# Performance work log

Measured on AMD Instinct MI355X. Metric: run time of the kernel, lower is better.

Reference implementation:

```python
import jax, jax.numpy as jnp
import numpy as np

N, E, D = 20000, 160000, 128   # nodes, edges, d_model
GH, HC = 4, 128                # TransformerConv heads, per-head channels (= out_channels)
MH = 4                         # temporal MHA heads
MC = D // MH                   # temporal MHA per-head dim
EPS = 1e-5


def layer_norm(x, g, b):
    mu = x.mean(-1, keepdims=True)
    var = ((x - mu) ** 2).mean(-1, keepdims=True)
    return (x - mu) * jax.lax.rsqrt(var + EPS) * g + b


def forward(x, temporal_encoding, gq_w, gq_b, gk_w, gk_b, gv_w, gv_b, gs_w, gs_b,
            mha_wq, mha_bq, mha_wk, mha_bk, mha_wv, mha_bv, mha_wo, mha_bo,
            ffn_w1, ffn_b1, ffn_w2, ffn_b2,
            ln1_g, ln1_b, ln2_g, ln2_b, ln3_g, ln3_b, edge_index):
    src, dst = edge_index[0], edge_index[1]
    n = x.shape[0]
    # --- TransformerConv(in=D, out=D, heads=GH, concat=False, root_weight=True) ---
    q = (x @ gq_w.T + gq_b).reshape(n, GH, HC)
    k = (x @ gk_w.T + gk_b).reshape(n, GH, HC)
    v = (x @ gv_w.T + gv_b).reshape(n, GH, HC)
    # per-edge attention logits: <q_i, k_j> / sqrt(out_channels), message j->i
    alpha = (q[dst] * k[src]).sum(-1) / jnp.sqrt(jnp.asarray(HC, x.dtype))  # [E, GH]
    # numerically-stable segment softmax over incoming edges of each dst node
    m = jax.ops.segment_max(alpha, dst, num_segments=n)                     # [N, GH]
    ex = jnp.exp(alpha - m[dst])
    den = jax.ops.segment_sum(ex, dst, num_segments=n)
    w = ex / den[dst]                                                       # [E, GH]
    agg = jax.ops.segment_sum(w[..., None] * v[src], dst, num_segments=n)  # [N, GH, HC]
    graph_out = agg.mean(1) + (x @ gs_w.T + gs_b)  # concat=False -> head mean; + root skip lin
    x1 = layer_norm(x + graph_out, ln1_g, ln1_b)   # dropout is identity at eval
    # --- temporal MHA: per-node query (len 1) attends to its temporal encoding (kv len 1) ---
    tq = (x1 @ mha_wq.T + mha_bq).reshape(n, MH, MC)
    tk = (temporal_encoding @ mha_wk.T + mha_bk).reshape(n, MH, MC)
    tv = (temporal_encoding @ mha_wv.T + mha_bv).reshape(n, MH, MC)
    scores = (tq * tk).sum(-1, keepdims=True) / jnp.sqrt(jnp.asarray(MC, x.dtype))  # [N, MH, 1]
    attn = jax.nn.softmax(scores, axis=-1)  # exactly ones (single kv position); kept for fidelity
    temp_out = (attn * tv).reshape(n, D) @ mha_wo.T + mha_bo
    x2 = layer_norm(x1 + temp_out, ln2_g, ln2_b)
    # --- FFN ---
    h = jax.nn.relu(x2 @ ffn_w1.T + ffn_b1)
    ffn_out = h @ ffn_w2.T + ffn_b2
    return layer_norm(x2 + ffn_out, ln3_g, ln3_b)


def setup_inputs() -> dict:
    ks = jax.random.split(jax.random.key(0), 16)
    s = 0.05
    def p(i, shape):
        return jax.random.normal(ks[i], shape, jnp.float32) * s
    z = lambda *sh: jnp.zeros(sh, jnp.float32)
    o = lambda *sh: jnp.ones(sh, jnp.float32)
    return {
        "x": p(0, (N, D)),
        "temporal_encoding": p(1, (N, D)),
        "gq_w": p(2, (GH * HC, D)), "gq_b": z(GH * HC),
        "gk_w": p(3, (GH * HC, D)), "gk_b": z(GH * HC),
        "gv_w": p(4, (GH * HC, D)), "gv_b": z(GH * HC),
        "gs_w": p(5, (D, D)), "gs_b": z(D),
        "mha_wq": p(6, (D, D)), "mha_bq": z(D),
        "mha_wk": p(7, (D, D)), "mha_bk": z(D),
        "mha_wv": p(8, (D, D)), "mha_bv": z(D),
        "mha_wo": p(9, (D, D)), "mha_bo": z(D),
        "ffn_w1": p(10, (4 * D, D)), "ffn_b1": z(4 * D),
        "ffn_w2": p(11, (D, 4 * D)), "ffn_b2": z(D),
        "ln1_g": o(D), "ln1_b": z(D),
        "ln2_g": o(D), "ln2_b": z(D),
        "ln3_g": o(D), "ln3_b": z(D),
        "edge_index": jax.random.randint(ks[12], (2, E), 0, N, jnp.int32),
    }


def reference(x, temporal_encoding, gq_w, gq_b, gk_w, gk_b, gv_w, gv_b, gs_w, gs_b,
              mha_wq, mha_bq, mha_wk, mha_bk, mha_wv, mha_bv, mha_wo, mha_bo,
              ffn_w1, ffn_b1, ffn_w2, ffn_b2,
              ln1_g, ln1_b, ln2_g, ln2_b, ln3_g, ln3_b, edge_index):
    return forward(x, temporal_encoding, gq_w, gq_b, gk_w, gk_b, gv_w, gv_b, gs_w, gs_b,
                   mha_wq, mha_bq, mha_wk, mha_bk, mha_wv, mha_bv, mha_wo, mha_bo,
                   ffn_w1, ffn_b1, ffn_w2, ffn_b2,
                   ln1_g, ln1_b, ln2_g, ln2_b, ln3_g, ln3_b, edge_index)
```

## Files before the change

kernel.cpp:

```cpp
#include <hip/hip_runtime.h>

#define NN 20000
#define EE 160000
#define DD 128
#define GHC 512
#define INV_SQRT_HC 0.08838834764831845f

typedef __attribute__((ext_vector_type(8))) short short8;
typedef __attribute__((ext_vector_type(4))) short short4v;
typedef __attribute__((ext_vector_type(4))) float float4v;
typedef __attribute__((ext_vector_type(2))) float float2v;
typedef __attribute__((ext_vector_type(4))) unsigned uint4v;
typedef __attribute__((ext_vector_type(2))) unsigned uint2v;

__device__ inline float bf2f(unsigned short u) {
    union { unsigned u; float f; } x; x.u = ((unsigned)u) << 16; return x.f;
}
__device__ inline unsigned short f2bf(float f) {
    union { float f; unsigned u; } x; x.f = f;
    unsigned u = x.u;
    unsigned r = (u + 0x7fffu + ((u >> 16) & 1u)) >> 16;
    return (unsigned short)r;
}

__device__ inline void stage16(const short8* gsrc, short8* ldst) {
    __builtin_amdgcn_global_load_lds(
        (const __attribute__((address_space(1))) void*)gsrc,
        (__attribute__((address_space(3))) void*)ldst, 16, 0, 0);
}

#if defined(__has_builtin)
#if __has_builtin(__builtin_amdgcn_cvt_pk_f32_fp8) && __has_builtin(__builtin_amdgcn_cvt_pk_fp8_f32)
#define HW_FP8 1
#endif
#endif
#ifndef HW_FP8
#define HW_FP8 0
#endif

#if !HW_FP8
__device__ inline unsigned char sw_enc_fp8(float f) {
    if (!(f == f)) return 0x7f;
    unsigned s = (f < 0.f) ? 0x80u : 0u;
    float a = fabsf(f);
    if (a >= 448.f) return (unsigned char)(s | 0x7e);
    if (a < 5.96046448e-8f) return (unsigned char)s;
    int e; frexpf(a, &e);
    int E = e - 1;
    if (E < -6) E = -6;
    float q = ldexpf(rintf(ldexpf(a, 3 - E)), E - 3);
    if (q == 0.f) return (unsigned char)s;
    union { float f; unsigned u; } x; x.f = q;
    int qe = (int)((x.u >> 23) & 0xff) - 127;
    if (qe < -6) {
        unsigned mant = (unsigned)rintf(ldexpf(q, 9));
        return (unsigned char)(s | mant);
    }
    unsigned mant = (x.u >> 20) & 7;
    int ebits = qe + 7;
    if (ebits > 15) { ebits = 15; mant = 6; }
    return (unsigned char)(s | ((unsigned)ebits << 3) | mant);
}
__device__ inline float sw_dec_fp8(unsigned char u) {
    unsigned s = u >> 7, e = (u >> 3) & 15, m = u & 7;
    float v = e ? ldexpf((float)(8 + m), (int)e - 10) : ldexpf((float)m, -9);
    return s ? -v : v;
}
#endif

__device__ inline unsigned short fp8_enc2(float a, float b) {
#if HW_FP8
    int r = __builtin_amdgcn_cvt_pk_fp8_f32(a, b, 0, false);
    return (unsigned short)(r & 0xffff);
#else
    return (unsigned short)(sw_enc_fp8(a) | ((unsigned)sw_enc_fp8(b) << 8));
#endif
}
__device__ inline float2v fp8_dec2_lo(unsigned w) {
#if HW_FP8
    return __builtin_amdgcn_cvt_pk_f32_fp8((int)w, false);
#else
    float2v r;
    r[0] = sw_dec_fp8((unsigned char)(w & 0xff));
    r[1] = sw_dec_fp8((unsigned char)((w >> 8) & 0xff));
    return r;
#endif
}
__device__ inline float2v fp8_dec2_hi(unsigned w) {
#if HW_FP8
    return __builtin_amdgcn_cvt_pk_f32_fp8((int)w, true);
#else
    float2v r;
    r[0] = sw_dec_fp8((unsigned char)((w >> 16) & 0xff));
    r[1] = sw_dec_fp8((unsigned char)(w >> 24));
    return r;
#endif
}

struct WPack { const void* in[18]; };
__device__ __constant__ const int WSZ[18] = {
    65536, 65536, 65536, 512, 512, 512,
    16384, 128, 65536, 512, 65536, 128,
    128, 128, 128, 128, 128, 128 };

__global__ void prep_kernel(const float* __restrict__ x, const float* __restrict__ te,
                            unsigned short* __restrict__ xcout, WPack p,
                            unsigned short* __restrict__ wcout,
                            const float* __restrict__ wv, const float* __restrict__ bv,
                            const float* __restrict__ wo, const float* __restrict__ bo,
                            unsigned short* __restrict__ wcomb,
                            unsigned short* __restrict__ bcomb,
                            const int* __restrict__ e_dst, int* __restrict__ counts)
{
    const int b = blockIdx.x;
    const int tid = threadIdx.x;
    if (b < 1024) {
        const long n4half = (long)NN * DD / 4;
        short4v* out4 = reinterpret_cast<short4v*>(xcout);
        long i = (long)b * 256 + tid;
        const long stride = 1024L * 256;
        const long tot = 2 * n4half;
        for (; i < tot; i += stride) {
            const float4v* src = (i < n4half)
                ? reinterpret_cast<const float4v*>(x)
                : reinterpret_cast<const float4v*>(te) - n4half;
            float4v v = src[i];
            short4v o;
            o[0] = (short)f2bf(v[0]); o[1] = (short)f2bf(v[1]);
            o[2] = (short)f2bf(v[2]); o[3] = (short)f2bf(v[3]);
            out4[i] = o;
        }
    } else if (b < 1600) {
        const int seg = (b - 1024) >> 5;
        const int rep = (b - 1024) & 31;
        int off = 0;
#pragma unroll
        for (int s = 0; s < 18; ++s) if (s < seg) off += WSZ[s];
        const int n = WSZ[seg];
        const float* q = (const float*)p.in[seg];
        for (int i = rep * 256 + tid; i < n; i += 32 * 256)
            wcout[off + i] = f2bf(q[i]);
    } else if (b < 1664) {
        int e = (b - 1600) * 256 + tid;
        int i = e >> 7, kk = e & 127;
        float s = 0.f;
        for (int j = 0; j < 128; ++j)
            s += wo[i * 128 + j] * wv[j * 128 + kk];
        wcomb[e] = f2bf(s);
        if (b == 1600 && tid < 128) {
            float t = 0.f;
            for (int j = 0; j < 128; ++j) t += wo[tid * 128 + j] * bv[j];
            bcomb[tid] = f2bf(t + bo[tid]);
        }
    } else {
        int e = (b - 1664) * 256 + tid;
        if (e < EE) {
            int d = e_dst[e];
            if (d >= 0 && d < NN) atomicAdd(&counts[d], 1);
        }
    }
}

__global__ __launch_bounds__(256) void gemm3_kernel(
    const unsigned short* __restrict__ A, const unsigned short* __restrict__ W,
    const unsigned short* __restrict__ bias, unsigned short* __restrict__ out,
    unsigned char* __restrict__ kvout, int M, int Nout, int split, int relu,
    int nxg, int ncol)
{
    __shared__ short8 wslab[2048];
    __shared__ __attribute__((aligned(16))) unsigned stile4[4][16][32];
    const int tid  = threadIdx.x;
    const int lane = tid & 63;
    const int wid  = tid >> 6;
    const int quad = lane >> 4;
    const int l15  = lane & 15;

    const int nb  = nxg * ncol;
    const int qq  = nb >> 3, rm = nb & 7;
    const int xcd = blockIdx.x & 7, slot = blockIdx.x >> 3;
    const int c   = (xcd < rm) ? xcd * (qq + 1) + slot
                               : rm * (qq + 1) + (xcd - rm) * qq + slot;
    const int xg = c / ncol;
    const int yg = c - xg * ncol;
    const int colbase0 = yg * 128;
    const int rowg = xg * 256;

    const bool isfp8 = (colbase0 >= split);
    const int kvcol = colbase0 - split;
    const int which = isfp8 ? (kvcol >> 9) : 0;
    const int head  = isfp8 ? ((kvcol & 511) >> 7) : 0;

    const short8* A8 = reinterpret_cast<const short8*>(A);
    const short8* W8 = reinterpret_cast<const short8*>(W);

    short8 a4[4];
    {
        int arow = rowg + wid * 16 + l15;
        if (arow >= M) arow = M - 1;
#pragma unroll
        for (int i = 0; i < 4; ++i) a4[i] = A8[(size_t)arow * 16 + i * 4 + quad];
    }

#pragma unroll
    for (int rep = 0; rep < 8; ++rep) {
        const int fi  = (rep * 4 + wid) & 3;
        const int ft  = rep & 3;
        const int ftt = rep >> 2;
        const int wrow = colbase0 + ftt * 64 + 16 * ft + l15;
        stage16(&W8[(size_t)wrow * 16 + fi * 4 + quad], &wslab[rep * 256 + wid * 64]);
    }

    float bvv[2][4];
#pragma unroll
    for (int tt = 0; tt < 2; ++tt)
#pragma unroll
        for (int t = 0; t < 4; ++t)
            bvv[tt][t] = bf2f(bias[colbase0 + tt * 64 + 16 * t + l15]);

    __syncthreads();

    unsigned short* fp = reinterpret_cast<unsigned short*>(&stile4[wid][0][0]);

#pragma unroll
    for (int tg = 0; tg < 4; ++tg) {
        const int rowbase = rowg + tg * 64 + wid * 16;

        short8 a4n[4];
        if (tg < 3) {
            int arow = rowbase + 64 + l15;
            if (arow >= M) arow = M - 1;
#pragma unroll
            for (int i = 0; i < 4; ++i) a4n[i] = A8[(size_t)arow * 16 + i * 4 + quad];
        }

#pragma unroll
        for (int tt = 0; tt < 2; ++tt) {
            float4v acc[4];
#pragma unroll
            for (int t = 0; t < 4; ++t) acc[t] = (float4v){0.f, 0.f, 0.f, 0.f};

#pragma unroll
            for (int i = 0; i < 4; ++i) {
#pragma unroll
                for (int t = 0; t < 4; ++t) {
                    short8 b = wslab[((tt * 4 + t) * 4 + i) * 64 + lane];
                    acc[t] = __builtin_amdgcn_mfma_f32_16x16x32_bf16(a4[i], b, acc[t], 0, 0, 0);
                }
            }

            if (!isfp8) {
#pragma unroll
                for (int t = 0; t < 4; ++t) {
#pragma unroll
                    for (int r = 0; r < 4; ++r) {
                        float vv = acc[t][r] + bvv[tt][t];
                        if (relu) vv = fmaxf(vv, 0.f);
                        float ov = __shfl_xor(vv, 1, 64);
                        if ((l15 & 1) == 0) {
                            const int row = quad * 4 + r;
                            const int cs  = (8 * t + (l15 >> 1)) ^ ((row & 7) << 2);
                            stile4[wid][row][cs] =
                                (unsigned)f2bf(vv) | ((unsigned)f2bf(ov) << 16);
                        }
                    }
                }
                const int rr0 = lane >> 3;
                const int cd  = (lane & 7) * 4;
#pragma unroll
                for (int it = 0; it < 2; ++it) {
                    int rw = rr0 + it * 8;
                    int grow = rowbase + rw;
                    if (grow < M) {
                        const int cs = cd ^ ((rw & 7) << 2);
                        uint4v v = *reinterpret_cast<const uint4v*>(&stile4[wid][rw][cs]);
                        *reinterpret_cast<uint4v*>(&out[(size_t)grow * Nout + colbase0 + tt * 64 + cd * 2]) = v;
                    }
                }
            } else {
#pragma unroll
                for (int t = 0; t < 4; ++t) {
#pragma unroll
                    for (int r = 0; r < 4; ++r) {
                        float vv = (acc[t][r] + bvv[tt][t]) * 256.f;
                        float ov = __shfl_xor(vv, 1, 64);
                        if ((l15 & 1) == 0) {
                            const int row = quad * 4 + r;
                            const int u = row * 64 + tt * 32 + 8 * t + (l15 >> 1);
                            fp[u ^ ((row & 7) << 3)] = fp8_enc2(vv, ov);
                        }
                    }
                }
            }
        }

        if (isfp8) {
#pragma unroll
            for (int it = 0; it < 2; ++it) {
                int u = lane + it * 64;
                int row = u >> 3;
                int part = u & 7;
                int grow = rowbase + row;
                if (grow < M) {
                    const int ui = (row * 64 + part * 8) ^ ((row & 7) << 3);
                    uint4v v = *reinterpret_cast<const uint4v*>(&fp[ui]);
                    size_t ro = (size_t)grow * 1024 + (size_t)which * 512
                              + (size_t)head * 128 + (size_t)part * 16;
                    *reinterpret_cast<uint4v*>(kvout + ro) = v;
                }
            }
        }

        if (tg < 3) {
#pragma unroll
            for (int i = 0; i < 4; ++i) a4[i] = a4n[i];
        }
    }
}

__global__ __launch_bounds__(256) void gemm_ln2_kernel(
    const unsigned short* __restrict__ A, const unsigned short* __restrict__ W,
    const unsigned short* __restrict__ bias,
    const float* __restrict__ residf, const float* __restrict__ c,
    const unsigned short* __restrict__ g, const unsigned short* __restrict__ beta,
    float* __restrict__ outf, unsigned short* __restrict__ outb, int M, int K)
{
    __shared__ short8 wslab[2048];
    __shared__ unsigned short stile[4][16][136];
    const int tid  = threadIdx.x;
    const int lane = tid & 63;
    const int wid  = tid >> 6;
    const int quad = lane >> 4;
    const int l15  = lane & 15;
    const int rowbase = blockIdx.x * 64 + wid * 16;

    int arow = rowbase + l15;
    if (arow >= M) arow = M - 1;

    const short8* A8 = reinterpret_cast<const short8*>(A);
    const short8* W8 = reinterpret_cast<const short8*>(W);
    const int k8 = K >> 3;
    const int kchunks = K >> 7;

    float4v acc[2][4];
#pragma unroll
    for (int tt = 0; tt < 2; ++tt)
#pragma unroll
        for (int t = 0; t < 4; ++t) acc[tt][t] = (float4v){0.f, 0.f, 0.f, 0.f};

    for (int cc = 0; cc < kchunks; ++cc) {
        if (cc > 0) __syncthreads();
#pragma unroll
        for (int rep = 0; rep < 8; ++rep) {
            const int fi  = (rep * 4 + wid) & 3;
            const int ft  = rep & 3;
            const int ftt = rep >> 2;
            const int wrow = ftt * 64 + 16 * ft + l15;
            stage16(&W8[(size_t)wrow * k8 + cc * 16 + fi * 4 + quad],
                    &wslab[rep * 256 + wid * 64]);
        }
        short8 a4[4];
#pragma unroll
        for (int i = 0; i < 4; ++i) a4[i] = A8[(size_t)arow * k8 + cc * 16 + i * 4 + quad];
        __syncthreads();
#pragma unroll
        for (int tt = 0; tt < 2; ++tt)
#pragma unroll
            for (int i = 0; i < 4; ++i)
#pragma unroll
                for (int t = 0; t < 4; ++t) {
                    short8 b = wslab[((tt * 4 + t) * 4 + i) * 64 + lane];
                    acc[tt][t] = __builtin_amdgcn_mfma_f32_16x16x32_bf16(a4[i], b, acc[tt][t], 0, 0, 0);
                }
    }

#pragma unroll
    for (int tt = 0; tt < 2; ++tt)
#pragma unroll
        for (int t = 0; t < 4; ++t) {
            float bv = bf2f(bias[tt * 64 + 16 * t + l15]);
#pragma unroll
            for (int r = 0; r < 4; ++r)
                stile[wid][quad * 4 + r][tt * 64 + 16 * t + l15] = f2bf(acc[tt][t][r] + bv);
        }

    const int r  = lane >> 2;
    const int p  = lane & 3;
    const int grow = rowbase + r;
    const int gr = (grow < M) ? grow : M - 1;

    float v[32];
    const short8* st8 = reinterpret_cast<const short8*>(&stile[wid][r][p * 32]);
#pragma unroll
    for (int q = 0; q < 4; ++q) {
        short8 sb = st8[q];
#pragma unroll
        for (int j = 0; j < 8; ++j) v[q * 8 + j] = bf2f((unsigned short)sb[j]);
    }
    const float4v* r4 = reinterpret_cast<const float4v*>(&residf[(size_t)gr * 128 + p * 32]);
#pragma unroll
    for (int q = 0; q < 8; ++q) {
        float4v rv = r4[q];
#pragma unroll
        for (int j = 0; j < 4; ++j) v[q * 4 + j] += rv[j];
    }
    if (c) {
        const float4v* c4 = reinterpret_cast<const float4v*>(&c[(size_t)gr * 128 + p * 32]);
#pragma unroll
        for (int q = 0; q < 8; ++q) {
            float4v cv = c4[q];
#pragma unroll
            for (int j = 0; j < 4; ++j) v[q * 4 + j] += cv[j];
        }
    }
    float s = 0.f, sq = 0.f;
#pragma unroll
    for (int i = 0; i < 32; ++i) { s += v[i]; sq += v[i] * v[i]; }
    s  += __shfl_xor(s, 1, 64);  s  += __shfl_xor(s, 2, 64);
    sq += __shfl_xor(sq, 1, 64); sq += __shfl_xor(sq, 2, 64);
    float mu  = s * (1.f / 128.f);
    float var = sq * (1.f / 128.f) - mu * mu;
    float rs  = rsqrtf(fmaxf(var, 0.f) + 1e-5f);

    if (grow < M) {
        const short8* g8 = reinterpret_cast<const short8*>(&g[p * 32]);
        const short8* b8 = reinterpret_cast<const short8*>(&beta[p * 32]);
        float o[32];
#pragma unroll
        for (int q = 0; q < 4; ++q) {
            short8 gg = g8[q], bb = b8[q];
#pragma unroll
            for (int j = 0; j < 8; ++j)
                o[q * 8 + j] = (v[q * 8 + j] - mu) * rs * bf2f((unsigned short)gg[j])
                               + bf2f((unsigned short)bb[j]);
        }
        float4v* o4 = reinterpret_cast<float4v*>(outf + (size_t)grow * 128 + p * 32);
#pragma unroll
        for (int q = 0; q < 8; ++q) {
            float4v ov = {o[q * 4], o[q * 4 + 1], o[q * 4 + 2], o[q * 4 + 3]};
            o4[q] = ov;
        }
        if (outb) {
            short8* ob8 = reinterpret_cast<short8*>(outb + (size_t)grow * 128 + p * 32);
#pragma unroll
            for (int q = 0; q < 4; ++q) {
                short8 oo;
#pragma unroll
                for (int j = 0; j < 8; ++j) oo[j] = (short)f2bf(o[q * 8 + j]);
                ob8[q] = oo;
            }
        }
    }
}

__global__ __launch_bounds__(256) void gemm_ln12_kernel(
    const unsigned short* __restrict__ A1, const unsigned short* __restrict__ W1,
    const unsigned short* __restrict__ b1,
    const float* __restrict__ rx, const float* __restrict__ ragg,
    const unsigned short* __restrict__ g1, const unsigned short* __restrict__ be1,
    const unsigned short* __restrict__ A2, const unsigned short* __restrict__ W2,
    const unsigned short* __restrict__ b2,
    const unsigned short* __restrict__ g2, const unsigned short* __restrict__ be2,
    float* __restrict__ outf, unsigned short* __restrict__ outb, int M)
{
    __shared__ short8 wslab[2048];
    __shared__ unsigned short stile[4][16][136];
    const int tid  = threadIdx.x;
    const int lane = tid & 63;
    const int wid  = tid >> 6;
    const int quad = lane >> 4;
    const int l15  = lane & 15;
    const int rowbase = blockIdx.x * 64 + wid * 16;

    int arow = rowbase + l15;
    if (arow >= M) arow = M - 1;

    const short8* A81 = reinterpret_cast<const short8*>(A1);
    const short8* A82 = reinterpret_cast<const short8*>(A2);
    const short8* W81 = reinterpret_cast<const short8*>(W1);
    const short8* W82 = reinterpret_cast<const short8*>(W2);

#pragma unroll
    for (int rep = 0; rep < 8; ++rep) {
        const int fi  = (rep * 4 + wid) & 3;
        const int ft  = rep & 3;
        const int ftt = rep >> 2;
        const int wrow = ftt * 64 + 16 * ft + l15;
        stage16(&W81[(size_t)wrow * 16 + fi * 4 + quad], &wslab[rep * 256 + wid * 64]);
    }
    short8 a4[4];
#pragma unroll
    for (int i = 0; i < 4; ++i) a4[i] = A81[(size_t)arow * 16 + i * 4 + quad];
    __syncthreads();

    float4v acc1[2][4];
#pragma unroll
    for (int tt = 0; tt < 2; ++tt)
#pragma unroll
        for (int t = 0; t < 4; ++t) acc1[tt][t] = (float4v){0.f, 0.f, 0.f, 0.f};
#pragma unroll
    for (int tt = 0; tt < 2; ++tt)
#pragma unroll
        for (int i = 0; i < 4; ++i)
#pragma unroll
            for (int t = 0; t < 4; ++t) {
                short8 b = wslab[((tt * 4 + t) * 4 + i) * 64 + lane];
                acc1[tt][t] = __builtin_amdgcn_mfma_f32_16x16x32_bf16(a4[i], b, acc1[tt][t], 0, 0, 0);
            }
    __syncthreads();

#pragma unroll
    for (int rep = 0; rep < 8; ++rep) {
        const int fi  = (rep * 4 + wid) & 3;
        const int ft  = rep & 3;
        const int ftt = rep >> 2;
        const int wrow = ftt * 64 + 16 * ft + l15;
        stage16(&W82[(size_t)wrow * 16 + fi * 4 + quad], &wslab[rep * 256 + wid * 64]);
    }
    short8 a42[4];
#pragma unroll
    for (int i = 0; i < 4; ++i) a42[i] = A82[(size_t)arow * 16 + i * 4 + quad];

#pragma unroll
    for (int tt = 0; tt < 2; ++tt)
#pragma unroll
        for (int t = 0; t < 4; ++t) {
            float bv = bf2f(b1[tt * 64 + 16 * t + l15]);
#pragma unroll
            for (int r = 0; r < 4; ++r)
                stile[wid][quad * 4 + r][tt * 64 + 16 * t + l15] = f2bf(acc1[tt][t][r] + bv);
        }

    const int r  = lane >> 2;
    const int p  = lane & 3;
    const int grow = rowbase + r;
    const int gr = (grow < M) ? grow : M - 1;

    float v[32];
    {
        const short8* st8 = reinterpret_cast<const short8*>(&stile[wid][r][p * 32]);
#pragma unroll
        for (int q = 0; q < 4; ++q) {
            short8 sb = st8[q];
#pragma unroll
            for (int j = 0; j < 8; ++j) v[q * 8 + j] = bf2f((unsigned short)sb[j]);
        }
        const float4v* r4 = reinterpret_cast<const float4v*>(&rx[(size_t)gr * 128 + p * 32]);
        const float4v* c4 = reinterpret_cast<const float4v*>(&ragg[(size_t)gr * 128 + p * 32]);
#pragma unroll
        for (int q = 0; q < 8; ++q) {
            float4v rv = r4[q];
            float4v cv = c4[q];
#pragma unroll
            for (int j = 0; j < 4; ++j) v[q * 4 + j] += rv[j] + cv[j];
        }
    }
    float x1[32];
    {
        float s = 0.f, sq = 0.f;
#pragma unroll
        for (int i = 0; i < 32; ++i) { s += v[i]; sq += v[i] * v[i]; }
        s  += __shfl_xor(s, 1, 64);  s  += __shfl_xor(s, 2, 64);
        sq += __shfl_xor(sq, 1, 64); sq += __shfl_xor(sq, 2, 64);
        float mu  = s * (1.f / 128.f);
        float var = sq * (1.f / 128.f) - mu * mu;
        float rs  = rsqrtf(fmaxf(var, 0.f) + 1e-5f);
        const short8* g8 = reinterpret_cast<const short8*>(&g1[p * 32]);
        const short8* b8 = reinterpret_cast<const short8*>(&be1[p * 32]);
#pragma unroll
        for (int q = 0; q < 4; ++q) {
            short8 gg = g8[q], bb = b8[q];
#pragma unroll
            for (int j = 0; j < 8; ++j)
                x1[q * 8 + j] = (v[q * 8 + j] - mu) * rs * bf2f((unsigned short)gg[j])
                                + bf2f((unsigned short)bb[j]);
        }
    }

    __syncthreads();

    float4v acc2[2][4];
#pragma unroll
    for (int tt = 0; tt < 2; ++tt)
#pragma unroll
        for (int t = 0; t < 4; ++t) acc2[tt][t] = (float4v){0.f, 0.f, 0.f, 0.f};
#pragma unroll
    for (int tt = 0; tt < 2; ++tt)
#pragma unroll
        for (int i = 0; i < 4; ++i)
#pragma unroll
            for (int t = 0; t < 4; ++t) {
                short8 b = wslab[((tt * 4 + t) * 4 + i) * 64 + lane];
                acc2[tt][t] = __builtin_amdgcn_mfma_f32_16x16x32_bf16(a42[i], b, acc2[tt][t], 0, 0, 0);
            }

#pragma unroll
    for (int tt = 0; tt < 2; ++tt)
#pragma unroll
        for (int t = 0; t < 4; ++t) {
            float bv = bf2f(b2[tt * 64 + 16 * t + l15]);
#pragma unroll
            for (int r2 = 0; r2 < 4; ++r2)
                stile[wid][quad * 4 + r2][tt * 64 + 16 * t + l15] = f2bf(acc2[tt][t][r2] + bv);
        }

    {
        const short8* st8 = reinterpret_cast<const short8*>(&stile[wid][r][p * 32]);
#pragma unroll
        for (int q = 0; q < 4; ++q) {
            short8 sb = st8[q];
#pragma unroll
            for (int j = 0; j < 8; ++j) v[q * 8 + j] = bf2f((unsigned short)sb[j]) + x1[q * 8 + j];
        }
    }
    float s = 0.f, sq = 0.f;
#pragma unroll
    for (int i = 0; i < 32; ++i) { s += v[i]; sq += v[i] * v[i]; }
    s  += __shfl_xor(s, 1, 64);  s  += __shfl_xor(s, 2, 64);
    sq += __shfl_xor(sq, 1, 64); sq += __shfl_xor(sq, 2, 64);
    float mu  = s * (1.f / 128.f);
    float var = sq * (1.f / 128.f) - mu * mu;
    float rs  = rsqrtf(fmaxf(var, 0.f) + 1e-5f);

    if (grow < M) {
        const short8* g8 = reinterpret_cast<const short8*>(&g2[p * 32]);
        const short8* b8 = reinterpret_cast<const short8*>(&be2[p * 32]);
        float o[32];
#pragma unroll
        for (int q = 0; q < 4; ++q) {
            short8 gg = g8[q], bb = b8[q];
#pragma unroll
            for (int j = 0; j < 8; ++j)
                o[q * 8 + j] = (v[q * 8 + j] - mu) * rs * bf2f((unsigned short)gg[j])
                               + bf2f((unsigned short)bb[j]);
        }
        float4v* o4 = reinterpret_cast<float4v*>(outf + (size_t)grow * 128 + p * 32);
#pragma unroll
        for (int q = 0; q < 8; ++q) {
            float4v ov = {o[q * 4], o[q * 4 + 1], o[q * 4 + 2], o[q * 4 + 3]};
            o4[q] = ov;
        }
        short8* ob8 = reinterpret_cast<short8*>(outb + (size_t)grow * 128 + p * 32);
#pragma unroll
        for (int q = 0; q < 4; ++q) {
            short8 oo;
#pragma unroll
            for (int j = 0; j < 8; ++j) oo[j] = (short)f2bf(o[q * 8 + j]);
            ob8[q] = oo;
        }
    }
}

__global__ __launch_bounds__(1024) void scan_kernel(
    const int* __restrict__ counts, int* __restrict__ offsets, int* __restrict__ pos, int n)
{
    __shared__ int wsum[16];
    __shared__ int carry_s;
    const int tid = threadIdx.x;
    const int wid = tid >> 6, lane = tid & 63;
    int vals[20];
#pragma unroll
    for (int cI = 0; cI < 20; ++cI) {
        int i = cI * 1024 + tid;
        vals[cI] = (i < n) ? counts[i] : 0;
    }
    if (tid == 0) carry_s = 0;
    __syncthreads();
#pragma unroll
    for (int cI = 0; cI < 20; ++cI) {
        int i = cI * 1024 + tid;
        int val = vals[cI];
        int x = val;
#pragma unroll
        for (int off = 1; off < 64; off <<= 1) {
            int t = __shfl_up(x, off, 64);
            if (lane >= off) x += t;
        }
        if (lane == 63) wsum[wid] = x;
        __syncthreads();
        if (wid == 0 && lane < 16) {
            int s = wsum[lane];
#pragma unroll
            for (int off = 1; off < 16; off <<= 1) {
                int t = __shfl_up(s, off, 64);
                if (lane >= off) s += t;
            }
            wsum[lane] = s;
        }
        __syncthreads();
        int prefix = (wid > 0 ? wsum[wid - 1] : 0) + carry_s;
        int ex = prefix + x - val;
        if (i < n) { offsets[i] = ex; pos[i] = ex; }
        __syncthreads();
        if (tid == 0) carry_s += wsum[15];
        __syncthreads();
    }
    if (tid == 0) offsets[n] = carry_s;
}

__global__ void scatter_kernel(const int* __restrict__ src, const int* __restrict__ dst,
                               int* __restrict__ pos, int* __restrict__ sorted_src, int E)
{
    int e = blockIdx.x * 256 + threadIdx.x;
    if (e < E) {
        int d = dst[e];
        if (d >= 0 && d < NN) {
            int p = atomicAdd(&pos[d], 1);
            if (p >= 0 && p < E) sorted_src[p] = src[e];
        }
    }
}

__device__ inline void agg_edge(const uint2v& kk, const uint2v& vv,
                                const float* qf, float* acc, float& ssum)
{
    float2v k01 = fp8_dec2_lo(kk[0]);
    float2v k23 = fp8_dec2_hi(kk[0]);
    float2v k45 = fp8_dec2_lo(kk[1]);
    float2v k67 = fp8_dec2_hi(kk[1]);
    float dot = qf[0] * k01[0] + qf[1] * k01[1] + qf[2] * k23[0] + qf[3] * k23[1]
              + qf[4] * k45[0] + qf[5] * k45[1] + qf[6] * k67[0] + qf[7] * k67[1];
    dot += __shfl_xor(dot, 1, 64);
    dot += __shfl_xor(dot, 2, 64);
    dot += __shfl_xor(dot, 4, 64);
    dot += __shfl_xor(dot, 8, 64);
    float pp = __expf(dot);
    ssum += pp;
    float2v v01 = fp8_dec2_lo(vv[0]);
    float2v v23 = fp8_dec2_hi(vv[0]);
    float2v v45 = fp8_dec2_lo(vv[1]);
    float2v v67 = fp8_dec2_hi(vv[1]);
    acc[0] += pp * v01[0]; acc[1] += pp * v01[1];
    acc[2] += pp * v23[0]; acc[3] += pp * v23[1];
    acc[4] += pp * v45[0]; acc[5] += pp * v45[1];
    acc[6] += pp * v67[0]; acc[7] += pp * v67[1];
}

__global__ __launch_bounds__(256) void agg_kernel(
    const unsigned short* __restrict__ q, const unsigned char* __restrict__ kvb,
    const int* __restrict__ offsets, const int* __restrict__ srcs,
    float* __restrict__ aggb)
{
    __shared__ float sacc[4][64][8];
    __shared__ float sssum[4][64];
    const int tid  = threadIdx.x;
    const int wid  = tid >> 6;
    const int lane = tid & 63;
    const int node = blockIdx.x * 2 + (wid >> 1);
    const int half = wid & 1;

    const short8* q8 = reinterpret_cast<const short8*>(q);
    const int fidx = (lane >> 4) * 16 + (lane & 15);
    const int koff = fidx * 8;

    short8 qv = q8[(size_t)node * 64 + fidx];
    float qf[8];
#pragma unroll
    for (int i = 0; i < 8; ++i)
        qf[i] = bf2f((unsigned short)qv[i]) * (INV_SQRT_HC / 256.f);

    int beg = offsets[node], end = offsets[node + 1];
    if (beg < 0) beg = 0;
    if (end > EE) end = EE;
    float ssum = 0.f;
    float acc[8];
#pragma unroll
    for (int i = 0; i < 8; ++i) acc[i] = 0.f;

    const int start = beg + half;
    int nce = (end > start) ? ((end - start + 1) >> 1) : 0;
    int ncap = (nce > 64) ? 64 : nce;

    int sv = 0;
    if (lane < ncap) {
        int s = srcs[start + 2 * lane];
        if (s < 0) s = 0;
        if (s >= NN) s = NN - 1;
        sv = s;
    }
    if (ncap > 0) {
        int s0 = __shfl(sv, 0, 64);
        uint2v kc = *reinterpret_cast<const uint2v*>(kvb + (size_t)s0 * 1024 + koff);
        uint2v vc = *reinterpret_cast<const uint2v*>(kvb + (size_t)s0 * 1024 + 512 + koff);
        for (int i = 0; i < ncap; ++i) {
            uint2v kn, vn;
            if (i + 1 < ncap) {
                int sn = __shfl(sv, i + 1, 64);
                kn = *reinterpret_cast<const uint2v*>(kvb + (size_t)sn * 1024 + koff);
                vn = *reinterpret_cast<const uint2v*>(kvb + (size_t)sn * 1024 + 512 + koff);
            }
            agg_edge(kc, vc, qf, acc, ssum);
            kc = kn; vc = vn;
        }
    }
    for (int j = start + 128; j < end; j += 2) {
        int s = srcs[j];
        if (s < 0) s = 0;
        if (s >= NN) s = NN - 1;
        uint2v kc = *reinterpret_cast<const uint2v*>(kvb + (size_t)s * 1024 + koff);
        uint2v vc = *reinterpret_cast<const uint2v*>(kvb + (size_t)s * 1024 + 512 + koff);
        agg_edge(kc, vc, qf, acc, ssum);
    }

#pragma unroll
    for (int i = 0; i < 8; ++i) sacc[wid][lane][i] = acc[i];
    sssum[wid][lane] = ssum;
    __syncthreads();
    if (half == 0) {
#pragma unroll
        for (int i = 0; i < 8; ++i) acc[i] += sacc[wid ^ 1][lane][i];
        ssum += sssum[wid ^ 1][lane];

        float inv = (ssum > 0.f) ? 1.f / (256.f * ssum) : 0.f;
#pragma unroll
        for (int i = 0; i < 8; ++i) acc[i] *= inv;
#pragma unroll
        for (int i = 0; i < 8; ++i) {
            acc[i] += __shfl_xor(acc[i], 16, 64);
            acc[i] += __shfl_xor(acc[i], 32, 64);
            acc[i] *= 0.25f;
        }
        if (lane < 16) {
            float4v* o = reinterpret_cast<float4v*>(aggb + (size_t)node * 128 + lane * 8);
            o[0] = (float4v){acc[0], acc[1], acc[2], acc[3]};
            o[1] = (float4v){acc[4], acc[5], acc[6], acc[7]};
        }
    }
}

extern "C" void kernel_launch(void* const* d_in, const int* in_sizes, int n_in,
                              void* d_out, int out_size, void* d_ws, size_t ws_size,
                              hipStream_t stream)
{
    const int* edge_index = (const int*)d_in[28];
    const int* e_src = edge_index;
    const int* e_dst = edge_index + EE;

    if (n_in < 29 || in_sizes[0] != NN * DD || in_sizes[28] != 2 * EE || out_size != NN * DD)
        return;

    const size_t SZ_OFF  = (size_t)(NN + 16) * 4;
    const size_t SZ_CNT  = (size_t)NN * 4;
    const size_t SZ_SS   = (size_t)EE * 4;
    const size_t SZ_SM   = (size_t)NN * DD * 2;
    const size_t SZ_F32  = (size_t)NN * DD * 4;
    const size_t SZ_Q    = (size_t)NN * 512 * 2;
    const size_t SZ_KV   = (size_t)NN * 1024;
    const size_t SZ_HB   = (size_t)NN * GHC * 2;
    const size_t WC_ELE  = 347136;
    const size_t SZ_WC   = WC_ELE * 2;
    const size_t SZ_WCB  = 16384 * 2 + 256;
    const size_t REQUIRED = SZ_OFF + 2 * SZ_CNT + SZ_SS + 2 * SZ_SM + SZ_WC + SZ_WCB
                          + SZ_Q + SZ_KV + 3 * SZ_F32 + SZ_SM + SZ_HB;

    if (ws_size < REQUIRED) return;

    char* w = (char*)d_ws;
    int* offsets = (int*)w;        w += SZ_OFF;
    int* counts  = (int*)w;        w += SZ_CNT;
    int* pos     = (int*)w;        w += SZ_CNT;
    int* sorted_src = (int*)w;     w += SZ_SS;
    unsigned short* xc   = (unsigned short*)w; w += SZ_SM;
    unsigned short* tec  = (unsigned short*)w; w += SZ_SM;
    unsigned short* wc   = (unsigned short*)w; w += SZ_WC;
    unsigned short* wcomb = (unsigned short*)w; w += 16384 * 2;
    unsigned short* bcomb = (unsigned short*)w; w += 256;
    unsigned short* qb   = (unsigned short*)w; w += SZ_Q;
    unsigned char*  kvb  = (unsigned char*)w;  w += SZ_KV;
    float*          aggb = (float*)w;          w += SZ_F32;
    float*          x1f  = (float*)w;          w += SZ_F32;
    float*          x2f  = (float*)w;          w += SZ_F32;
    unsigned short* x2b  = (unsigned short*)w; w += SZ_SM;
    unsigned short* hbuf = (unsigned short*)w; w += SZ_HB;
    (void)x1f;

    unsigned short* cw = wc;
    unsigned short* qkv_w = cw; cw += 3 * 65536;
    unsigned short* qkv_b = cw; cw += 3 * 512;
    unsigned short* gs_w  = cw; cw += 16384;  unsigned short* gs_b  = cw; cw += 128;
    unsigned short* ffn_w1 = cw; cw += 65536; unsigned short* ffn_b1 = cw; cw += 512;
    unsigned short* ffn_w2 = cw; cw += 65536; unsigned short* ffn_b2 = cw; cw += 128;
    unsigned short* ln1_g = cw; cw += 128;    unsigned short* ln1_b = cw; cw += 128;
    unsigned short* ln2_g = cw; cw += 128;    unsigned short* ln2_b = cw; cw += 128;
    unsigned short* ln3_g = cw; cw += 128;    unsigned short* ln3_b = cw; cw += 128;

    const int EB = (EE + 255) / 256;
    const dim3 blk(256);
    const int MB = (NN + 63) / 64;
    const int MB2 = (NN + 255) / 256;

    WPack pack;
    const int live_idx[18] = {2,4,6, 3,5,7, 8,9, 18,19, 20,21, 22,23,24,25,26,27};
    for (int i = 0; i < 18; ++i) pack.in[i] = d_in[live_idx[i]];

    (void)hipMemsetAsync(counts, 0, SZ_CNT, stream);
    prep_kernel<<<1664 + EB, blk, 0, stream>>>((const float*)d_in[0], (const float*)d_in[1],
                                               xc, pack, wc,
                                               (const float*)d_in[14], (const float*)d_in[15],
                                               (const float*)d_in[16], (const float*)d_in[17],
                                               wcomb, bcomb, e_dst, counts);

    scan_kernel<<<1, 1024, 0, stream>>>(counts, offsets, pos, NN);
    scatter_kernel<<<EB, blk, 0, stream>>>(e_src, e_dst, pos, sorted_src, EE);

    gemm3_kernel<<<dim3(MB2 * 12), blk, 0, stream>>>(xc, qkv_w, qkv_b, qb, kvb,
                                                     NN, 512, 512, 0, MB2, 12);
    agg_kernel<<<NN / 2, blk, 0, stream>>>(qb, kvb, offsets, sorted_src, aggb);
    gemm_ln12_kernel<<<MB, blk, 0, stream>>>(xc, gs_w, gs_b,
                                             (const float*)d_in[0], aggb,
                                             ln1_g, ln1_b,
                                             tec, wcomb, bcomb,
                                             ln2_g, ln2_b, x2f, x2b, NN);
    gemm3_kernel<<<dim3(MB2 * 4), blk, 0, stream>>>(x2b, ffn_w1, ffn_b1, hbuf, nullptr,
                                                    NN, 512, 99999, 1, MB2, 4);
    gemm_ln2_kernel<<<MB, blk, 0, stream>>>(hbuf, ffn_w2, ffn_b2, x2f, nullptr,
                                            ln3_g, ln3_b, (float*)d_out, nullptr, NN, GHC);
}
```

Before: 288.0 us.

## Swap MFMA operands so accumulators hold row-major output, dropping LDS transposes

Swaps the A/B operands of the bf16 MFMA in the GEMM kernels so each lane's accumulator holds four consecutive output columns of one row. The LayerNorm epilogues can then run straight from registers using cross-quad shuffles, with no staging through an LDS tile, and the fp32 intermediate is no longer rounded to bf16. The projection epilogues write packed bf16 via v_cvt_pk_bf16_f32, or four fp8 values per dword, with vectorised bias loads, which removes per-element shuffles and half-lane stores. The cost is strided 16-byte global residual loads and stores per lane instead of contiguous 128-byte row chunks, plus inline asm that assumes the target supports v_cvt_pk_bf16_f32.

```diff
diff --git a/kernel.cpp b/kernel.cpp
--- a/kernel.cpp
+++ b/kernel.cpp
@@ -21,6 +21,11 @@
     unsigned u = x.u;
     unsigned r = (u + 0x7fffu + ((u >> 16) & 1u)) >> 16;
     return (unsigned short)r;
+}
+__device__ inline unsigned cvt_pk_bf16(float a, float b) {
+    unsigned d;
+    asm("v_cvt_pk_bf16_f32 %0, %1, %2" : "=v"(d) : "v"(a), "v"(b));
+    return d;
 }
 
 __device__ inline void stage16(const short8* gsrc, short8* ldst) {
@@ -68,12 +73,14 @@
 }
 #endif
 
-__device__ inline unsigned short fp8_enc2(float a, float b) {
+__device__ inline unsigned fp8_enc4(float a, float b, float c, float d) {
 #if HW_FP8
     int r = __builtin_amdgcn_cvt_pk_fp8_f32(a, b, 0, false);
-    return (unsigned short)(r & 0xffff);
+    r = __builtin_amdgcn_cvt_pk_fp8_f32(c, d, r, true);
+    return (unsigned)r;
 #else
-    return (unsigned short)(sw_enc_fp8(a) | ((unsigned)sw_enc_fp8(b) << 8));
+    return (unsigned)sw_enc_fp8(a) | ((unsigned)sw_enc_fp8(b) << 8)
+         | ((unsigned)sw_enc_fp8(c) << 16) | ((unsigned)sw_enc_fp8(d) << 24);
 #endif
 }
 __device__ inline float2v fp8_dec2_lo(unsigned w) {
@@ -210,16 +217,17 @@
         stage16(&W8[(size_t)wrow * 16 + fi * 4 + quad], &wslab[rep * 256 + wid * 64]);
     }
 
-    float bvv[2][4];
+    short4v bs4[2][4];
 #pragma unroll
     for (int tt = 0; tt < 2; ++tt)
 #pragma unroll
         for (int t = 0; t < 4; ++t)
-            bvv[tt][t] = bf2f(bias[colbase0 + tt * 64 + 16 * t + l15]);
+            bs4[tt][t] = *reinterpret_cast<const short4v*>(
+                &bias[colbase0 + tt * 64 + 16 * t + quad * 4]);
 
     __syncthreads();
 
-    unsigned short* fp = reinterpret_cast<unsigned short*>(&stile4[wid][0][0]);
+    unsigned* fpd = &stile4[wid][0][0];
 
 #pragma unroll
     for (int tg = 0; tg < 4; ++tg) {
@@ -243,26 +251,25 @@
             for (int i = 0; i < 4; ++i) {
 #pragma unroll
                 for (int t = 0; t < 4; ++t) {
-                    short8 b = wslab[((tt * 4 + t) * 4 + i) * 64 + lane];
-                    acc[t] = __builtin_amdgcn_mfma_f32_16x16x32_bf16(a4[i], b, acc[t], 0, 0, 0);
+                    short8 wb = wslab[((tt * 4 + t) * 4 + i) * 64 + lane];
+                    acc[t] = __builtin_amdgcn_mfma_f32_16x16x32_bf16(wb, a4[i], acc[t], 0, 0, 0);
                 }
             }
 
             if (!isfp8) {
 #pragma unroll
                 for (int t = 0; t < 4; ++t) {
-#pragma unroll
-                    for (int r = 0; r < 4; ++r) {
-                        float vv = acc[t][r] + bvv[tt][t];
-                        if (relu) vv = fmaxf(vv, 0.f);
-                        float ov = __shfl_xor(vv, 1, 64);
-                        if ((l15 & 1) == 0) {
-                            const int row = quad * 4 + r;
-                            const int cs  = (8 * t + (l15 >> 1)) ^ ((row & 7) << 2);
-                            stile4[wid][row][cs] =
-                                (unsigned)f2bf(vv) | ((unsigned)f2bf(ov) << 16);
-                        }
+                    float v0 = acc[t][0] + bf2f((unsigned short)bs4[tt][t][0]);
+                    float v1 = acc[t][1] + bf2f((unsigned short)bs4[tt][t][1]);
+                    float v2 = acc[t][2] + bf2f((unsigned short)bs4[tt][t][2]);
+                    float v3 = acc[t][3] + bf2f((unsigned short)bs4[tt][t][3]);
+                    if (relu) {
+                        v0 = fmaxf(v0, 0.f); v1 = fmaxf(v1, 0.f);
+                        v2 = fmaxf(v2, 0.f); v3 = fmaxf(v3, 0.f);
                     }
+                    uint2v d = { cvt_pk_bf16(v0, v1), cvt_pk_bf16(v2, v3) };
+                    const int dc = (8 * t + quad * 2) ^ ((l15 & 7) << 2);
+                    *reinterpret_cast<uint2v*>(&stile4[wid][l15][dc]) = d;
                 }
                 const int rr0 = lane >> 3;
                 const int cd  = (lane & 7) * 4;
@@ -279,16 +286,12 @@
             } else {
 #pragma unroll
                 for (int t = 0; t < 4; ++t) {
-#pragma unroll
-                    for (int r = 0; r < 4; ++r) {
-                        float vv = (acc[t][r] + bvv[tt][t]) * 256.f;
-                        float ov = __shfl_xor(vv, 1, 64);
-                        if ((l15 & 1) == 0) {
-                            const int row = quad * 4 + r;
-                            const int u = row * 64 + tt * 32 + 8 * t + (l15 >> 1);
-                            fp[u ^ ((row & 7) << 3)] = fp8_enc2(vv, ov);
-                        }
-                    }
+                    float v0 = (acc[t][0] + bf2f((unsigned short)bs4[tt][t][0])) * 256.f;
+                    float v1 = (acc[t][1] + bf2f((unsigned short)bs4[tt][t][1])) * 256.f;
+                    float v2 = (acc[t][2] + bf2f((unsigned short)bs4[tt][t][2])) * 256.f;
+                    float v3 = (acc[t][3] + bf2f((unsigned short)bs4[tt][t][3])) * 256.f;
+                    const int dc = (tt * 16 + 4 * t + quad) ^ ((l15 & 7) << 2);
+                    fpd[l15 * 32 + dc] = fp8_enc4(v0, v1, v2, v3);
                 }
             }
         }
@@ -301,8 +304,8 @@
                 int part = u & 7;
                 int grow = rowbase + row;
                 if (grow < M) {
-                    const int ui = (row * 64 + part * 8) ^ ((row & 7) << 3);
-                    uint4v v = *reinterpret_cast<const uint4v*>(&fp[ui]);
+                    const int db = row * 32 + ((part * 4) ^ ((row & 7) << 2));
+                    uint4v v = *reinterpret_cast<const uint4v*>(&fpd[db]);
                     size_t ro = (size_t)grow * 1024 + (size_t)which * 512
                               + (size_t)head * 128 + (size_t)part * 16;
                     *reinterpret_cast<uint4v*>(kvout + ro) = v;
@@ -325,7 +328,6 @@
     float* __restrict__ outf, unsigned short* __restrict__ outb, int M, int K)
 {
     __shared__ short8 wslab[2048];
-    __shared__ unsigned short stile[4][16][136];
     const int tid  = threadIdx.x;
     const int lane = tid & 63;
     const int wid  = tid >> 6;
@@ -333,8 +335,8 @@
     const int l15  = lane & 15;
     const int rowbase = blockIdx.x * 64 + wid * 16;
 
-    int arow = rowbase + l15;
-    if (arow >= M) arow = M - 1;
+    const int grow = rowbase + l15;
+    const int gr = (grow < M) ? grow : M - 1;
 
     const short8* A8 = reinterpret_cast<const short8*>(A);
     const short8* W8 = reinterpret_cast<const short8*>(W);
@@ -360,7 +362,7 @@
         }
         short8 a4[4];
 #pragma unroll
-        for (int i = 0; i < 4; ++i) a4[i] = A8[(size_t)arow * k8 + cc * 16 + i * 4 + quad];
+        for (int i = 0; i < 4; ++i) a4[i] = A8[(size_t)gr * k8 + cc * 16 + i * 4 + quad];
         __syncthreads();
 #pragma unroll
         for (int tt = 0; tt < 2; ++tt)
@@ -368,87 +370,63 @@
             for (int i = 0; i < 4; ++i)
 #pragma unroll
                 for (int t = 0; t < 4; ++t) {
-                    short8 b = wslab[((tt * 4 + t) * 4 + i) * 64 + lane];
-                    acc[tt][t] = __builtin_amdgcn_mfma_f32_16x16x32_bf16(a4[i], b, acc[tt][t], 0, 0, 0);
+                    short8 wb = wslab[((tt * 4 + t) * 4 + i) * 64 + lane];
+                    acc[tt][t] = __builtin_amdgcn_mfma_f32_16x16x32_bf16(wb, a4[i], acc[tt][t], 0, 0, 0);
                 }
     }
 
+    float v[32];
 #pragma unroll
     for (int tt = 0; tt < 2; ++tt)
 #pragma unroll
         for (int t = 0; t < 4; ++t) {
-            float bv = bf2f(bias[tt * 64 + 16 * t + l15]);
+            const int n0 = tt * 64 + 16 * t + quad * 4;
+            short4v bs = *reinterpret_cast<const short4v*>(&bias[n0]);
+            float4v rv = *reinterpret_cast<const float4v*>(&residf[(size_t)gr * 128 + n0]);
 #pragma unroll
             for (int r = 0; r < 4; ++r)
-                stile[wid][quad * 4 + r][tt * 64 + 16 * t + l15] = f2bf(acc[tt][t][r] + bv);
-        }
-
-    const int r  = lane >> 2;
-    const int p  = lane & 3;
-    const int grow = rowbase + r;
-    const int gr = (grow < M) ? grow : M - 1;
-
-    float v[32];
-    const short8* st8 = reinterpret_cast<const short8*>(&stile[wid][r][p * 32]);
-#pragma unroll
-    for (int q = 0; q < 4; ++q) {
-        short8 sb = st8[q];
-#pragma unroll
-        for (int j = 0; j < 8; ++j) v[q * 8 + j] = bf2f((unsigned short)sb[j]);
-    }
-    const float4v* r4 = reinterpret_cast<const float4v*>(&residf[(size_t)gr * 128 + p * 32]);
-#pragma unroll
-    for (int q = 0; q < 8; ++q) {
-        float4v rv = r4[q];
-#pragma unroll
-        for (int j = 0; j < 4; ++j) v[q * 4 + j] += rv[j];
-    }
+                v[(tt * 4 + t) * 4 + r] = acc[tt][t][r]
+                    + bf2f((unsigned short)bs[r]) + rv[r];
+        }
     if (c) {
-        const float4v* c4 = reinterpret_cast<const float4v*>(&c[(size_t)gr * 128 + p * 32]);
-#pragma unroll
-        for (int q = 0; q < 8; ++q) {
-            float4v cv = c4[q];
-#pragma unroll
-            for (int j = 0; j < 4; ++j) v[q * 4 + j] += cv[j];
-        }
+#pragma unroll
+        for (int tt = 0; tt < 2; ++tt)
+#pragma unroll
+            for (int t = 0; t < 4; ++t) {
+                const int n0 = tt * 64 + 16 * t + quad * 4;
+                float4v cv = *reinterpret_cast<const float4v*>(&c[(size_t)gr * 128 + n0]);
+#pragma unroll
+                for (int r = 0; r < 4; ++r) v[(tt * 4 + t) * 4 + r] += cv[r];
+            }
     }
     float s = 0.f, sq = 0.f;
 #pragma unroll
     for (int i = 0; i < 32; ++i) { s += v[i]; sq += v[i] * v[i]; }
-    s  += __shfl_xor(s, 1, 64);  s  += __shfl_xor(s, 2, 64);
-    sq += __shfl_xor(sq, 1, 64); sq += __shfl_xor(sq, 2, 64);
+    s  += __shfl_xor(s, 16, 64);  s  += __shfl_xor(s, 32, 64);
+    sq += __shfl_xor(sq, 16, 64); sq += __shfl_xor(sq, 32, 64);
     float mu  = s * (1.f / 128.f);
     float var = sq * (1.f / 128.f) - mu * mu;
     float rs  = rsqrtf(fmaxf(var, 0.f) + 1e-5f);
 
     if (grow < M) {
-        const short8* g8 = reinterpret_cast<const short8*>(&g[p * 32]);
-        const short8* b8 = reinterpret_cast<const short8*>(&beta[p * 32]);
-        float o[32];
-#pragma unroll
-        for (int q = 0; q < 4; ++q) {
-            short8 gg = g8[q], bb = b8[q];
-#pragma unroll
-            for (int j = 0; j < 8; ++j)
-                o[q * 8 + j] = (v[q * 8 + j] - mu) * rs * bf2f((unsigned short)gg[j])
-                               + bf2f((unsigned short)bb[j]);
-        }
-        float4v* o4 = reinterpret_cast<float4v*>(outf + (size_t)grow * 128 + p * 32);
-#pragma unroll
-        for (int q = 0; q < 8; ++q) {
-            float4v ov = {o[q * 4], o[q * 4 + 1], o[q * 4 + 2], o[q * 4 + 3]};
-            o4[q] = ov;
-        }
-        if (outb) {
-            short8* ob8 = reinterpret_cast<short8*>(outb + (size_t)grow * 128 + p * 32);
-#pragma unroll
-            for (int q = 0; q < 4; ++q) {
-                short8 oo;
-#pragma unroll
-                for (int j = 0; j < 8; ++j) oo[j] = (short)f2bf(o[q * 8 + j]);
-                ob8[q] = oo;
-            }
-        }
+#pragma unroll
+        for (int tt = 0; tt < 2; ++tt)
+#pragma unroll
+            for (int t = 0; t < 4; ++t) {
+                const int n0 = tt * 64 + 16 * t + quad * 4;
+                short4v gg = *reinterpret_cast<const short4v*>(&g[n0]);
+                short4v bb = *reinterpret_cast<const short4v*>(&beta[n0]);
+                float4v ov;
+#pragma unroll
+                for (int r = 0; r < 4; ++r)
+                    ov[r] = (v[(tt * 4 + t) * 4 + r] - mu) * rs
+                            * bf2f((unsigned short)gg[r]) + bf2f((unsigned short)bb[r]);
+                *reinterpret_cast<float4v*>(&outf[(size_t)grow * 128 + n0]) = ov;
+                if (outb) {
+                    uint2v d = { cvt_pk_bf16(ov[0], ov[1]), cvt_pk_bf16(ov[2], ov[3]) };
+                    *reinterpret_cast<uint2v*>(&outb[(size_t)grow * 128 + n0]) = d;
+                }
+            }
     }
 }
 
@@ -463,7 +441,6 @@
     float* __restrict__ outf, unsigned short* __restrict__ outb, int M)
 {
     __shared__ short8 wslab[2048];
-    __shared__ unsigned short stile[4][16][136];
     const int tid  = threadIdx.x;
     const int lane = tid & 63;
     const int wid  = tid >> 6;
@@ -471,8 +448,8 @@
     const int l15  = lane & 15;
     const int rowbase = blockIdx.x * 64 + wid * 16;
 
-    int arow = rowbase + l15;
-    if (arow >= M) arow = M - 1;
+    const int grow = rowbase + l15;
+    const int gr = (grow < M) ? grow : M - 1;
 
     const short8* A81 = reinterpret_cast<const short8*>(A1);
     const short8* A82 = reinterpret_cast<const short8*>(A2);
@@ -489,7 +466,7 @@
     }
     short8 a4[4];
 #pragma unroll
-    for (int i = 0; i < 4; ++i) a4[i] = A81[(size_t)arow * 16 + i * 4 + quad];
+    for (int i = 0; i < 4; ++i) a4[i] = A81[(size_t)gr * 16 + i * 4 + quad];
     __syncthreads();
 
     float4v acc1[2][4];
@@ -503,8 +480,8 @@
         for (int i = 0; i < 4; ++i)
 #pragma unroll
             for (int t = 0; t < 4; ++t) {
-                short8 b = wslab[((tt * 4 + t) * 4 + i) * 64 + lane];
-                acc1[tt][t] = __builtin_amdgcn_mfma_f32_16x16x32_bf16(a4[i], b, acc1[tt][t], 0, 0, 0);
+                short8 wb = wslab[((tt * 4 + t) * 4 + i) * 64 + lane];
+                acc1[tt][t] = __builtin_amdgcn_mfma_f32_16x16x32_bf16(wb, a4[i], acc1[tt][t], 0, 0, 0);
             }
     __syncthreads();
 
@@ -518,62 +495,44 @@
     }
     short8 a42[4];
 #pragma unroll
-    for (int i = 0; i < 4; ++i) a42[i] = A82[(size_t)arow * 16 + i * 4 + quad];
-
-#pragma unroll
-    for (int tt = 0; tt < 2; ++tt)
-#pragma unroll
-        for (int t = 0; t < 4; ++t) {
-            float bv = bf2f(b1[tt * 64 + 16 * t + l15]);
-#pragma unroll
-            for (int r = 0; r < 4; ++r)
-                stile[wid][quad * 4 + r][tt * 64 + 16 * t + l15] = f2bf(acc1[tt][t][r] + bv);
-        }
-
-    const int r  = lane >> 2;
-    const int p  = lane & 3;
-    const int grow = rowbase + r;
-    const int gr = (grow < M) ? grow : M - 1;
-
-    float v[32];
-    {
-        const short8* st8 = reinterpret_cast<const short8*>(&stile[wid][r][p * 32]);
-#pragma unroll
-        for (int q = 0; q < 4; ++q) {
-            short8 sb = st8[q];
-#pragma unroll
-            for (int j = 0; j < 8; ++j) v[q * 8 + j] = bf2f((unsigned short)sb[j]);
-        }
-        const float4v* r4 = reinterpret_cast<const float4v*>(&rx[(size_t)gr * 128 + p * 32]);
-        const float4v* c4 = reinterpret_cast<const float4v*>(&ragg[(size_t)gr * 128 + p * 32]);
-#pragma unroll
-        for (int q = 0; q < 8; ++q) {
-            float4v rv = r4[q];
-            float4v cv = c4[q];
-#pragma unroll
-            for (int j = 0; j < 4; ++j) v[q * 4 + j] += rv[j] + cv[j];
-        }
-    }
+    for (int i = 0; i < 4; ++i) a42[i] = A82[(size_t)gr * 16 + i * 4 + quad];
+
     float x1[32];
     {
+        float v[32];
+#pragma unroll
+        for (int tt = 0; tt < 2; ++tt)
+#pragma unroll
+            for (int t = 0; t < 4; ++t) {
+                const int n0 = tt * 64 + 16 * t + quad * 4;
+                short4v bs = *reinterpret_cast<const short4v*>(&b1[n0]);
+                float4v rv = *reinterpret_cast<const float4v*>(&rx[(size_t)gr * 128 + n0]);
+                float4v cv = *reinterpret_cast<const float4v*>(&ragg[(size_t)gr * 128 + n0]);
+#pragma unroll
+                for (int r = 0; r < 4; ++r)
+                    v[(tt * 4 + t) * 4 + r] = acc1[tt][t][r]
+                        + bf2f((unsigned short)bs[r]) + rv[r] + cv[r];
+            }
         float s = 0.f, sq = 0.f;
 #pragma unroll
         for (int i = 0; i < 32; ++i) { s += v[i]; sq += v[i] * v[i]; }
-        s  += __shfl_xor(s, 1, 64);  s  += __shfl_xor(s, 2, 64);
-        sq += __shfl_xor(sq, 1, 64); sq += __shfl_xor(sq, 2, 64);
+        s  += __shfl_xor(s, 16, 64);  s  += __shfl_xor(s, 32, 64);
+        sq += __shfl_xor(sq, 16, 64); sq += __shfl_xor(sq, 32, 64);
         float mu  = s * (1.f / 128.f);
         float var = sq * (1.f / 128.f) - mu * mu;
         float rs  = rsqrtf(fmaxf(var, 0.f) + 1e-5f);
-        const short8* g8 = reinterpret_cast<const short8*>(&g1[p * 32]);
-        const short8* b8 = reinterpret_cast<const short8*>(&be1[p * 32]);
-#pragma unroll
-        for (int q = 0; q < 4; ++q) {
-            short8 gg = g8[q], bb = b8[q];
-#pragma unroll
-            for (int j = 0; j < 8; ++j)
-                x1[q * 8 + j] = (v[q * 8 + j] - mu) * rs * bf2f((unsigned short)gg[j])
-                                + bf2f((unsigned short)bb[j]);
-        }
+#pragma unroll
+        for (int tt = 0; tt < 2; ++tt)
+#pragma unroll
+            for (int t = 0; t < 4; ++t) {
+                const int n0 = tt * 64 + 16 * t + quad * 4;
+                short4v gg = *reinterpret_cast<const short4v*>(&g1[n0]);
+                short4v bb = *reinterpret_cast<const short4v*>(&be1[n0]);
+#pragma unroll
+                for (int r = 0; r < 4; ++r)
+                    x1[(tt * 4 + t) * 4 + r] = (v[(tt * 4 + t) * 4 + r] - mu) * rs
+                        * bf2f((unsigned short)gg[r]) + bf2f((unsigned short)bb[r]);
+            }
     }
 
     __syncthreads();
@@ -589,64 +548,48 @@
         for (int i = 0; i < 4; ++i)
 #pragma unroll
             for (int t = 0; t < 4; ++t) {
-                short8 b = wslab[((tt * 4 + t) * 4 + i) * 64 + lane];
-                acc2[tt][t] = __builtin_amdgcn_mfma_f32_16x16x32_bf16(a42[i], b, acc2[tt][t], 0, 0, 0);
-            }
-
+                short8 wb = wslab[((tt * 4 + t) * 4 + i) * 64 + lane];
+                acc2[tt][t] = __builtin_amdgcn_mfma_f32_16x16x32_bf16(wb, a42[i], acc2[tt][t], 0, 0, 0);
+            }
+
+    float v[32];
 #pragma unroll
     for (int tt = 0; tt < 2; ++tt)
 #pragma unroll
         for (int t = 0; t < 4; ++t) {
-            float bv = bf2f(b2[tt * 64 + 16 * t + l15]);
-#pragma unroll
-            for (int r2 = 0; r2 < 4; ++r2)
-                stile[wid][quad * 4 + r2][tt * 64 + 16 * t + l15] = f2bf(acc2[tt][t][r2] + bv);
-        }
-
-    {
-        const short8* st8 = reinterpret_cast<const short8*>(&stile[wid][r][p * 32]);
-#pragma unroll
-        for (int q = 0; q < 4; ++q) {
-            short8 sb = st8[q];
-#pragma unroll
-            for (int j = 0; j < 8; ++j) v[q * 8 + j] = bf2f((unsigned short)sb[j]) + x1[q * 8 + j];
-        }
-    }
+            const int n0 = tt * 64 + 16 * t + quad * 4;
+            short4v bs = *reinterpret_cast<const short4v*>(&b2[n0]);
+#pragma unroll
+            for (int r = 0; r < 4; ++r)
+                v[(tt * 4 + t) * 4 + r] = acc2[tt][t][r]
+                    + bf2f((unsigned short)bs[r]) + x1[(tt * 4 + t) * 4 + r];
+        }
     float s = 0.f, sq = 0.f;
 #pragma unroll
     for (int i = 0; i < 32; ++i) { s += v[i]; sq += v[i] * v[i]; }
-    s  += __shfl_xor(s, 1, 64);  s  += __shfl_xor(s, 2, 64);
-    sq += __shfl_xor(sq, 1, 64); sq += __shfl_xor(sq, 2, 64);
+    s  += __shfl_xor(s, 16, 64);  s  += __shfl_xor(s, 32, 64);
+    sq += __shfl_xor(sq, 16, 64); sq += __shfl_xor(sq, 32, 64);
     float mu  = s * (1.f / 128.f);
     float var = sq * (1.f / 128.f) - mu * mu;
     float rs  = rsqrtf(fmaxf(var, 0.f) + 1e-5f);
 
     if (grow < M) {
-        const short8* g8 = reinterpret_cast<const short8*>(&g2[p * 32]);
-        const short8* b8 = reinterpret_cast<const short8*>(&be2[p * 32]);
-        float o[32];
-#pragma unroll
-        for (int q = 0; q < 4; ++q) {
-            short8 gg = g8[q], bb = b8[q];
-#pragma unroll
-            for (int j = 0; j < 8; ++j)
-                o[q * 8 + j] = (v[q * 8 + j] - mu) * rs * bf2f((unsigned short)gg[j])
-                               + bf2f((unsigned short)bb[j]);
-        }
-        float4v* o4 = reinterpret_cast<float4v*>(outf + (size_t)grow * 128 + p * 32);
-#pragma unroll
-        for (int q = 0; q < 8; ++q) {
-            float4v ov = {o[q * 4], o[q * 4 + 1], o[q * 4 + 2], o[q * 4 + 3]};
-            o4[q] = ov;
-        }
-        short8* ob8 = reinterpret_cast<short8*>(outb + (size_t)grow * 128 + p * 32);
-#pragma unroll
-        for (int q = 0; q < 4; ++q) {
-            short8 oo;
-#pragma unroll
-            for (int j = 0; j < 8; ++j) oo[j] = (short)f2bf(o[q * 8 + j]);
-            ob8[q] = oo;
-        }
+#pragma unroll
+        for (int tt = 0; tt < 2; ++tt)
+#pragma unroll
+            for (int t = 0; t < 4; ++t) {
+                const int n0 = tt * 64 + 16 * t + quad * 4;
+                short4v gg = *reinterpret_cast<const short4v*>(&g2[n0]);
+                short4v bb = *reinterpret_cast<const short4v*>(&be2[n0]);
+                float4v ov;
+#pragma unroll
+                for (int r = 0; r < 4; ++r)
+                    ov[r] = (v[(tt * 4 + t) * 4 + r] - mu) * rs
+                            * bf2f((unsigned short)gg[r]) + bf2f((unsigned short)bb[r]);
+                *reinterpret_cast<float4v*>(&outf[(size_t)grow * 128 + n0]) = ov;
+                uint2v d = { cvt_pk_bf16(ov[0], ov[1]), cvt_pk_bf16(ov[2], ov[3]) };
+                *reinterpret_cast<uint2v*>(&outb[(size_t)grow * 128 + n0]) = d;
+            }
     }
 }
 
```

Result: faster. 258.4 us (-10.3%).
